# Performance work log

Hardware: AMD Instinct MI355X
Metric: run time of the kernel (lower is better)

## Reference

```python
import jax, jax.numpy as jnp
import numpy as np

POLY_DEGREE = 3
LOW, MID, HIGH = 3, 6, 9
K = LOW + MID + HIGH  # 18 total harmonics
NUM_POINTS = 128 ** 3
BATCH = 4


def _band_sum(t, a, b, omega):
    """sum_k a_k*cos(w_k t) + b_k*sin(w_k t) without materializing [B,N,K].
    t: [B,N]; a,b: [N,k]; omega: [k]. Scans over the small harmonic axis."""
    def step(acc, xs):
        a_k, b_k, w = xs  # a_k,b_k: [N], w: scalar
        ph = w * t  # [B,N]
        return acc + a_k[None, :] * jnp.cos(ph) + b_k[None, :] * jnp.sin(ph), None
    acc0 = jnp.zeros_like(t)
    acc, _ = jax.lax.scan(step, acc0, (a.T, b.T, omega))
    return acc


def setup_inputs() -> dict:
    key = jax.random.key(0)
    k1, k2, k3, k4 = jax.random.split(key, 4)
    input_t = jax.random.uniform(k1, (BATCH,), dtype=jnp.float32)  # times in [0,1)
    poly_coeffs = jax.random.normal(k2, (NUM_POINTS, POLY_DEGREE + 1), dtype=jnp.float32) * 0.1
    fourier_a = jax.random.normal(k3, (NUM_POINTS, K), dtype=jnp.float32) * 0.1
    fourier_b = jax.random.normal(k4, (NUM_POINTS, K), dtype=jnp.float32) * 0.1
    return {
        "input_t": input_t,
        "poly_coeffs": poly_coeffs,
        "fourier_a": fourier_a,
        "fourier_b": fourier_b,
        "model_stage": 3,
    }


def reference(input_t, poly_coeffs, fourier_a, fourier_b, model_stage):
    B = input_t.shape[0]
    N = poly_coeffs.shape[0]
    t = jnp.broadcast_to(input_t[:, None], (B, N))  # [B, N]
    curr_stage = min(model_stage, 3) if model_stage >= 0 else 3
    omega = 2.0 * jnp.pi * jnp.arange(1, K + 1, dtype=jnp.float32)

    y_poly = jnp.zeros((B, N), dtype=jnp.float32)
    if POLY_DEGREE > 0 and curr_stage >= 0:
        for i in range(POLY_DEGREE + 1):
            y_poly = y_poly + poly_coeffs[:, i][None, :] * t ** i

    y_fourier = jnp.zeros((B, N), dtype=jnp.float32)
    bands = [(0, LOW, 1), (LOW, LOW + MID, 2), (LOW + MID, K, 3)]
    for s, e, req_stage in bands:
        if e > s and curr_stage >= req_stage:
            y_fourier = y_fourier + _band_sum(
                t, fourier_a[:, s:e], fourier_b[:, s:e], omega[s:e]
            )
    return y_poly, y_fourier
```

## Files before the change

### kernel.cpp

```cpp
#include <hip/hip_runtime.h>

#define KH 18
#define NPTS (128*128*128)
#define BB 4
#define BLK 256
#define TILE (BLK * KH)

__global__ __launch_bounds__(BLK, 4) void dddm_kernel(
    const float* __restrict__ input_t,
    const float* __restrict__ poly,
    const float* __restrict__ fa,
    const float* __restrict__ fb,
    const int*   __restrict__ stage_p,
    float* __restrict__ out)
{
    __shared__ float s[2 * TILE];
    __shared__ float seedT[BB], seedC[BB], seedS[BB];

    const int tid = threadIdx.x;
    const int n0  = blockIdx.x * BLK;
    const int n   = n0 + tid;

    if (tid < BB) {
        const float t = input_t[tid];
        float sn, cs;
        sincosf(6.283185307179586f * t, &sn, &cs);
        seedT[tid] = t; seedC[tid] = cs; seedS[tid] = sn;
    }

    const float4* fa4 = reinterpret_cast<const float4*>(fa + (size_t)n0 * KH);
    const float4* fb4 = reinterpret_cast<const float4*>(fb + (size_t)n0 * KH);
    float4* s4 = reinterpret_cast<float4*>(s);

    float4 v[9];
#pragma unroll
    for (int j = 0; j < 9; ++j) {
        const int idx = j * BLK + tid;
        v[j] = (idx < TILE / 4) ? fa4[idx] : fb4[idx - TILE / 4];
    }
#pragma unroll
    for (int j = 0; j < 9; ++j) {
        const int idx = j * BLK + tid;
        s4[idx] = v[j];
    }

    const int ms = *stage_p;
    const int cs_ = (ms >= 0) ? (ms < 3 ? ms : 3) : 3;
    const int kmax = (cs_ >= 3) ? 18 : (cs_ == 2 ? 9 : (cs_ == 1 ? 3 : 0));

    __syncthreads();

    const float4 c4 = reinterpret_cast<const float4*>(poly)[n];
    float d[BB], cc[BB], ss[BB], cp[BB], sp[BB], yp[BB], yf[BB];
#pragma unroll
    for (int b = 0; b < BB; ++b) {
        const float t  = seedT[b];
        const float c1 = seedC[b];
        const float s1 = seedS[b];
        yp[b] = ((c4.w * t + c4.z) * t + c4.y) * t + c4.x;
        cc[b] = c1; ss[b] = s1;
        cp[b] = 1.0f; sp[b] = 0.0f;
        d[b]  = 2.0f * c1;
        yf[b] = 0.0f;
    }

    const float2* ar = reinterpret_cast<const float2*>(s + tid * KH);
    const float2* br = reinterpret_cast<const float2*>(s + TILE + tid * KH);

    if (kmax == KH) {
#pragma unroll
        for (int j = 0; j < 9; ++j) {
            const float2 a2 = ar[j];
            const float2 b2 = br[j];
#pragma unroll
            for (int u = 0; u < 2; ++u) {
                const float ak = u ? a2.y : a2.x;
                const float bk = u ? b2.y : b2.x;
#pragma unroll
                for (int b = 0; b < BB; ++b) {
                    yf[b] = __builtin_fmaf(ak, cc[b], yf[b]);
                    yf[b] = __builtin_fmaf(bk, ss[b], yf[b]);
                    const float cn = __builtin_fmaf(d[b], cc[b], -cp[b]);
                    const float sn = __builtin_fmaf(d[b], ss[b], -sp[b]);
                    cp[b] = cc[b]; cc[b] = cn;
                    sp[b] = ss[b]; ss[b] = sn;
                }
            }
        }
    } else if (kmax > 0) {
        for (int k = 0; k < kmax; ++k) {
            const float ak = s[tid * KH + k];
            const float bk = s[TILE + tid * KH + k];
#pragma unroll
            for (int b = 0; b < BB; ++b) {
                yf[b] = __builtin_fmaf(ak, cc[b], yf[b]);
                yf[b] = __builtin_fmaf(bk, ss[b], yf[b]);
                const float cn = __builtin_fmaf(d[b], cc[b], -cp[b]);
                const float sn = __builtin_fmaf(d[b], ss[b], -sp[b]);
                cp[b] = cc[b]; cc[b] = cn;
                sp[b] = ss[b]; ss[b] = sn;
            }
        }
    }

#pragma unroll
    for (int b = 0; b < BB; ++b) {
        out[(size_t)b * NPTS + n]        = yp[b];
        out[(size_t)(BB + b) * NPTS + n] = yf[b];
    }
}

extern "C" void kernel_launch(void* const* d_in, const int* in_sizes, int n_in,
                              void* d_out, int out_size, void* d_ws, size_t ws_size,
                              hipStream_t stream) {
    const float* input_t = (const float*)d_in[0];
    const float* poly    = (const float*)d_in[1];
    const float* fa      = (const float*)d_in[2];
    const float* fb      = (const float*)d_in[3];
    const int*   stage   = (const int*)d_in[4];
    float* out = (float*)d_out;

    dddm_kernel<<<NPTS / BLK, BLK, 0, stream>>>(input_t, poly, fa, fb, stage, out);
}
```

Measured before the change: 349.2 us.

## Make kernel persistent with double-buffered async global-to-LDS tile prefetch

The one-block-per-256-point-tile launch becomes 512 persistent blocks, each looping over 16 tiles. The next tile's Fourier coefficients and poly coefficients are prefetched into a second LDS buffer with global_load_lds direct-to-LDS loads while the current tile is computed. The aim is to overlap HBM reads with compute and to stop staging through registers. In exchange, LDS use per block roughly doubles, launch bounds drop to 2 blocks per CU, and correctness depends on the end-of-iteration barrier also waiting for the async loads to finish.

```diff
diff --git a/kernel.cpp b/kernel.cpp
--- a/kernel.cpp
+++ b/kernel.cpp
@@ -4,9 +4,16 @@
 #define NPTS (128*128*128)
 #define BB 4
 #define BLK 256
-#define TILE (BLK * KH)
+#define NTILES (NPTS / BLK)
+#define NBLK 512
+#define TPB (NTILES / NBLK)
+#define TILE_A (BLK * KH)
+#define BUF_FLOATS (2 * TILE_A + BLK * 4)
 
-__global__ __launch_bounds__(BLK, 4) void dddm_kernel(
+typedef const __attribute__((address_space(1))) void* gp1_t;
+typedef __attribute__((address_space(3)))       void* lp3_t;
+
+__global__ __launch_bounds__(BLK, 2) void dddm_kernel(
     const float* __restrict__ input_t,
     const float* __restrict__ poly,
     const float* __restrict__ fa,
@@ -14,34 +21,41 @@
     const int*   __restrict__ stage_p,
     float* __restrict__ out)
 {
-    __shared__ float s[2 * TILE];
-    __shared__ float seedT[BB], seedC[BB], seedS[BB];
+    __shared__ __align__(16) float s[2 * BUF_FLOATS];
 
-    const int tid = threadIdx.x;
-    const int n0  = blockIdx.x * BLK;
-    const int n   = n0 + tid;
+    const int tid   = threadIdx.x;
+    const int wv    = tid >> 6;
+    const int lane  = tid & 63;
+    const int tile0 = blockIdx.x * TPB;
 
-    if (tid < BB) {
-        const float t = input_t[tid];
+    auto stage = [&](int t, int buf) {
+        const size_t f0 = (size_t)(tile0 + t) * TILE_A;
+        const float* ga = fa   + f0;
+        const float* gb = fb   + f0;
+        const float* gp = poly + (size_t)(tile0 + t) * (BLK * 4);
+        float* lb = s + buf * BUF_FLOATS;
+#pragma unroll
+        for (int r = 0; r < 10; ++r) {
+            const int c = wv * 10 + r;
+            const float* src;
+            if (c < 18)      src = ga + c * 256        + lane * 4;
+            else if (c < 36) src = gb + (c - 18) * 256 + lane * 4;
+            else             src = gp + (c - 36) * 256 + lane * 4;
+            __builtin_amdgcn_global_load_lds((gp1_t)src, (lp3_t)(lb + c * 256),
+                                             16, 0, 0);
+        }
+    };
+
+    stage(0, 0);
+
+    float tb[BB], c1[BB], s1[BB], dd[BB];
+#pragma unroll
+    for (int b = 0; b < BB; ++b) {
+        const float t = input_t[b];
+        tb[b] = t;
         float sn, cs;
         sincosf(6.283185307179586f * t, &sn, &cs);
-        seedT[tid] = t; seedC[tid] = cs; seedS[tid] = sn;
-    }
-
-    const float4* fa4 = reinterpret_cast<const float4*>(fa + (size_t)n0 * KH);
-    const float4* fb4 = reinterpret_cast<const float4*>(fb + (size_t)n0 * KH);
-    float4* s4 = reinterpret_cast<float4*>(s);
-
-    float4 v[9];
-#pragma unroll
-    for (int j = 0; j < 9; ++j) {
-        const int idx = j * BLK + tid;
-        v[j] = (idx < TILE / 4) ? fa4[idx] : fb4[idx - TILE / 4];
-    }
-#pragma unroll
-    for (int j = 0; j < 9; ++j) {
-        const int idx = j * BLK + tid;
-        s4[idx] = v[j];
+        c1[b] = cs; s1[b] = sn; dd[b] = 2.0f * cs;
     }
 
     const int ms = *stage_p;
@@ -50,63 +64,69 @@
 
     __syncthreads();
 
-    const float4 c4 = reinterpret_cast<const float4*>(poly)[n];
-    float d[BB], cc[BB], ss[BB], cp[BB], sp[BB], yp[BB], yf[BB];
+    for (int t = 0; t < TPB; ++t) {
+        if (t + 1 < TPB) stage(t + 1, (t + 1) & 1);
+
+        const float* sb = s + (t & 1) * BUF_FLOATS;
+
+        const float4 c4 = reinterpret_cast<const float4*>(sb + 2 * TILE_A)[tid];
+        float yp[BB], yf[BB], cc[BB], ss[BB], cp[BB], sp[BB];
 #pragma unroll
-    for (int b = 0; b < BB; ++b) {
-        const float t  = seedT[b];
-        const float c1 = seedC[b];
-        const float s1 = seedS[b];
-        yp[b] = ((c4.w * t + c4.z) * t + c4.y) * t + c4.x;
-        cc[b] = c1; ss[b] = s1;
-        cp[b] = 1.0f; sp[b] = 0.0f;
-        d[b]  = 2.0f * c1;
-        yf[b] = 0.0f;
-    }
+        for (int b = 0; b < BB; ++b) {
+            const float t0 = tb[b];
+            yp[b] = ((c4.w * t0 + c4.z) * t0 + c4.y) * t0 + c4.x;
+            cc[b] = c1[b]; ss[b] = s1[b];
+            cp[b] = 1.0f;  sp[b] = 0.0f;
+            yf[b] = 0.0f;
+        }
 
-    const float2* ar = reinterpret_cast<const float2*>(s + tid * KH);
-    const float2* br = reinterpret_cast<const float2*>(s + TILE + tid * KH);
+        const float2* ar = reinterpret_cast<const float2*>(sb + tid * KH);
+        const float2* br = reinterpret_cast<const float2*>(sb + TILE_A + tid * KH);
 
-    if (kmax == KH) {
+        if (kmax == KH) {
 #pragma unroll
-        for (int j = 0; j < 9; ++j) {
-            const float2 a2 = ar[j];
-            const float2 b2 = br[j];
+            for (int j = 0; j < 9; ++j) {
+                const float2 a2 = ar[j];
+                const float2 b2 = br[j];
 #pragma unroll
-            for (int u = 0; u < 2; ++u) {
-                const float ak = u ? a2.y : a2.x;
-                const float bk = u ? b2.y : b2.x;
+                for (int u = 0; u < 2; ++u) {
+                    const float ak = u ? a2.y : a2.x;
+                    const float bk = u ? b2.y : b2.x;
+#pragma unroll
+                    for (int b = 0; b < BB; ++b) {
+                        yf[b] = __builtin_fmaf(ak, cc[b], yf[b]);
+                        yf[b] = __builtin_fmaf(bk, ss[b], yf[b]);
+                        const float cn = __builtin_fmaf(dd[b], cc[b], -cp[b]);
+                        const float sn = __builtin_fmaf(dd[b], ss[b], -sp[b]);
+                        cp[b] = cc[b]; cc[b] = cn;
+                        sp[b] = ss[b]; ss[b] = sn;
+                    }
+                }
+            }
+        } else if (kmax > 0) {
+            for (int k = 0; k < kmax; ++k) {
+                const float ak = sb[tid * KH + k];
+                const float bk = sb[TILE_A + tid * KH + k];
 #pragma unroll
                 for (int b = 0; b < BB; ++b) {
                     yf[b] = __builtin_fmaf(ak, cc[b], yf[b]);
                     yf[b] = __builtin_fmaf(bk, ss[b], yf[b]);
-                    const float cn = __builtin_fmaf(d[b], cc[b], -cp[b]);
-                    const float sn = __builtin_fmaf(d[b], ss[b], -sp[b]);
+                    const float cn = __builtin_fmaf(dd[b], cc[b], -cp[b]);
+                    const float sn = __builtin_fmaf(dd[b], ss[b], -sp[b]);
                     cp[b] = cc[b]; cc[b] = cn;
                     sp[b] = ss[b]; ss[b] = sn;
                 }
             }
         }
-    } else if (kmax > 0) {
-        for (int k = 0; k < kmax; ++k) {
-            const float ak = s[tid * KH + k];
-            const float bk = s[TILE + tid * KH + k];
+
+        const int n = (tile0 + t) * BLK + tid;
 #pragma unroll
-            for (int b = 0; b < BB; ++b) {
-                yf[b] = __builtin_fmaf(ak, cc[b], yf[b]);
-                yf[b] = __builtin_fmaf(bk, ss[b], yf[b]);
-                const float cn = __builtin_fmaf(d[b], cc[b], -cp[b]);
-                const float sn = __builtin_fmaf(d[b], ss[b], -sp[b]);
-                cp[b] = cc[b]; cc[b] = cn;
-                sp[b] = ss[b]; ss[b] = sn;
-            }
+        for (int b = 0; b < BB; ++b) {
+            out[(size_t)b * NPTS + n]        = yp[b];
+            out[(size_t)(BB + b) * NPTS + n] = yf[b];
         }
-    }
 
-#pragma unroll
-    for (int b = 0; b < BB; ++b) {
-        out[(size_t)b * NPTS + n]        = yp[b];
-        out[(size_t)(BB + b) * NPTS + n] = yf[b];
+        __syncthreads();
     }
 }
 
@@ -120,5 +140,5 @@
     const int*   stage   = (const int*)d_in[4];
     float* out = (float*)d_out;
 
-    dddm_kernel<<<NPTS / BLK, BLK, 0, stream>>>(input_t, poly, fa, fb, stage, out);
+    dddm_kernel<<<NBLK, BLK, 0, stream>>>(input_t, poly, fa, fb, stage, out);
 }
```

Result: no change. 354.6 us (+1.6%).
